# Performance work log

Hardware: AMD Instinct MI355X
Metric: run time of the kernel (lower is better)

The kernel has to match this reference:

```python
import jax, jax.numpy as jnp
import numpy as np

EPS = 1e-06        # normalize eps and log eps (module's self.eps)
PDIST_EPS = 1e-06  # torch.nn.PairwiseDistance default eps: ||x1 - x2 + eps||_2

A, C, F = 4096, 8, 64


def setup_inputs() -> dict:
    key = jax.random.key(0)
    x = jax.random.normal(key, (A, C, F), dtype=jnp.float32)
    return {"x": x}


def reference(x) -> jnp.ndarray:
    a = x.shape[0]
    c = x.shape[1]
    # F.normalize(p=2, dim=-1, eps=EPS): x / max(||x||_2, eps)
    nrm = jnp.linalg.norm(x, axis=-1, keepdims=True)
    xn = x / jnp.maximum(nrm, EPS)
    # pairwise cosine similarity per group: [C, A, A]
    sim = jnp.einsum('acf,bcf->cab', xn, xn)
    # mask self-similarity on the diagonal with -1
    diag = jnp.eye(a, dtype=bool)[None, :, :]
    sim = jnp.where(diag, -1.0, sim)
    # nearest neighbor per (c, a): argmax over b -> [C, A] -> [A, C]
    idx = jnp.argmax(sim, axis=-1).T
    # gather matched embeddings: x_match[a, c, f] = xn[idx[a, c], c, f]
    x_match = xn[idx, jnp.arange(c)[None, :], :]
    # PairwiseDistance(p=2, eps=1e-6): ||x - x_match + eps||_2 over last dim
    min_dist = jnp.linalg.norm(xn - x_match + PDIST_EPS, axis=-1)
    loss = -jnp.mean(jnp.log(min_dist + EPS))
    return loss
```

## Files before the change

kernel.cpp:

```cpp
#include <hip/hip_runtime.h>
#include <math.h>

#define AN 4096
#define CN 8
#define FN 64
#define ACN (AN*CN)

typedef __attribute__((ext_vector_type(8))) short bf16x8;
typedef __attribute__((ext_vector_type(4))) float f32x4;

#define GLL16(gsrc, ldst) \
    __builtin_amdgcn_global_load_lds( \
        (const __attribute__((address_space(1))) void*)(gsrc), \
        (__attribute__((address_space(3))) void*)(ldst), 16, 0, 0)

__device__ inline unsigned short f2bf(float f) {
    unsigned u = __float_as_uint(f);
    unsigned r = ((u >> 16) & 1) + 0x7FFFu;
    return (unsigned short)((u + r) >> 16);
}

__global__ __launch_bounds__(256) void k1_normalize(const float* __restrict__ x,
                                                    unsigned short* __restrict__ xnb,
                                                    float* __restrict__ inv)
{
    int tid  = threadIdx.x;
    int grp  = tid >> 4;
    int slot = tid & 15;
    #pragma unroll
    for (int s = 0; s < 4; ++s) {
        int V = blockIdx.x * 64 + s * 16 + grp;
        const float4 v = *(const float4*)(x + (size_t)V * FN + slot * 4);
        float ss = v.x*v.x + v.y*v.y + v.z*v.z + v.w*v.w;
        ss += __shfl_xor(ss, 1);
        ss += __shfl_xor(ss, 2);
        ss += __shfl_xor(ss, 4);
        ss += __shfl_xor(ss, 8);
        float sc = 1.0f / fmaxf(sqrtf(ss), 1e-6f);
        int a = V >> 3, c = V & 7;
        ushort4 ob;
        ob.x = f2bf(v.x * sc); ob.y = f2bf(v.y * sc);
        ob.z = f2bf(v.z * sc); ob.w = f2bf(v.w * sc);
        *(ushort4*)(xnb + ((size_t)c * AN + a) * FN + slot * 4) = ob;
        if (slot == 0) inv[V] = sc;
    }
}

__global__ __launch_bounds__(256, 2) void k2_argmax(const unsigned short* __restrict__ xnb,
                                                    unsigned int* __restrict__ pP)
{
    __shared__ uint4 lds4[3 * 1024];

    int blk  = blockIdx.x;
    int half = blk & 1;
    int rt   = (blk >> 1) & 31;
    int c    = blk >> 6;
    int a0   = rt * 128;
    int b0base = half * 2048;

    const char* __restrict__ Xc = (const char*)(xnb + (size_t)c * AN * FN);

    int tid  = threadIdx.x;
    int lane = tid & 63;
    int w    = tid >> 6;
    int l15  = lane & 15;
    int quad = lane >> 4;

    int srow  = lane >> 3;
    int sslot = lane & 7;

    #pragma unroll
    for (int s = 0; s < 4; ++s) {
        int base = (w * 4 + s) * 64;
        int row  = (base >> 3) + srow;
        int gch  = sslot ^ (row & 7);
        size_t gb = (size_t)row * 128 + (size_t)gch * 16;
        GLL16(Xc + (size_t)(a0) * 128 + gb,      lds4 + base);
        GLL16(Xc + (size_t)(b0base) * 128 + gb,  lds4 + 1024 + base);
    }
    __syncthreads();

    bf16x8 afr[8][2];
    #pragma unroll
    for (int mi = 0; mi < 8; ++mi)
        #pragma unroll
        for (int ks = 0; ks < 2; ++ks) {
            int r  = mi * 16 + l15;
            int ch = (ks * 4 + quad) ^ (r & 7);
            afr[mi][ks] = ((const bf16x8*)lds4)[r * 8 + ch];
        }

    float bestp[32];
    #pragma unroll
    for (int i = 0; i < 32; ++i) bestp[i] = 0.0f;

    const f32x4 two = {2.0f, 2.0f, 2.0f, 2.0f};

    for (int it = 0; it < 16; ++it) {
        int cur = it & 1;

        if (it < 15) {
            int g0 = b0base + (it + 1) * 128;
            #pragma unroll
            for (int s = 0; s < 4; ++s) {
                int base = (w * 4 + s) * 64;
                int row  = (base >> 3) + srow;
                int gch  = sslot ^ (row & 7);
                GLL16(Xc + (size_t)(g0 + row) * 128 + (size_t)gch * 16,
                      lds4 + 1024 + (cur ^ 1) * 1024 + base);
            }
        }

        f32x4 acc[8][2];
        const bf16x8* bt = (const bf16x8*)(lds4 + 1024 + cur * 1024);
        #pragma unroll
        for (int ks = 0; ks < 2; ++ks) {
            #pragma unroll
            for (int ni = 0; ni < 2; ++ni) {
                int r  = w * 32 + ni * 16 + l15;
                int ch = (ks * 4 + quad) ^ (r & 7);
                bf16x8 bfr = bt[r * 8 + ch];
                #pragma unroll
                for (int mi = 0; mi < 8; ++mi)
                    acc[mi][ni] = __builtin_amdgcn_mfma_f32_16x16x32_bf16(
                        afr[mi][ks], bfr, (ks == 0) ? two : acc[mi][ni], 0, 0, 0);
            }
        }

        int colblk = b0base + it * 128 + w * 32;
        #pragma unroll
        for (int mi = 0; mi < 8; ++mi) {
            int rfrag = a0 + mi * 16;
            #pragma unroll
            for (int r = 0; r < 4; ++r) {
                unsigned p0 = (__float_as_uint(acc[mi][0][r]) & 0xFFFFF000u)
                            | (unsigned)(colblk + l15);
                unsigned p1 = (__float_as_uint(acc[mi][1][r]) & 0xFFFFF000u)
                            | (unsigned)(colblk + 16 + l15);
                float c0 = __uint_as_float(p0);
                float c1 = __uint_as_float(p1);
                if (rfrag == colblk) {
                    if (l15 == quad * 4 + r) c0 = 0.0f;
                }
                if (rfrag == colblk + 16) {
                    if (l15 == quad * 4 + r) c1 = 0.0f;
                }
                int bi = mi * 4 + r;
                bestp[bi] = fmaxf(fmaxf(c0, c1), bestp[bi]);
            }
        }

        __syncthreads();
    }

    #pragma unroll
    for (int i = 0; i < 32; ++i) {
        float v = bestp[i];
        v = fmaxf(v, __shfl_xor(v, 1));
        v = fmaxf(v, __shfl_xor(v, 2));
        v = fmaxf(v, __shfl_xor(v, 4));
        v = fmaxf(v, __shfl_xor(v, 8));
        bestp[i] = v;
    }
    __syncthreads();
    float* red = (float*)lds4;
    if (l15 == 0) {
        #pragma unroll
        for (int mi = 0; mi < 8; ++mi)
            #pragma unroll
            for (int r = 0; r < 4; ++r)
                red[w * 128 + mi * 16 + quad * 4 + r] = bestp[mi * 4 + r];
    }
    __syncthreads();
    if (tid < 128) {
        float p = fmaxf(fmaxf(red[tid], red[128 + tid]),
                        fmaxf(red[256 + tid], red[384 + tid]));
        int a = a0 + tid;
        pP[(size_t)half * ACN + (size_t)a * CN + c] = __float_as_uint(p);
    }
}

__global__ __launch_bounds__(256) void k3_dist(const float* __restrict__ x,
                                               const float* __restrict__ inv,
                                               const unsigned int* __restrict__ pP,
                                               float* __restrict__ partials)
{
    int tid = threadIdx.x;
    int id = blockIdx.x * 256 + tid;
    float p0 = __uint_as_float(pP[id]);
    float p1 = __uint_as_float(pP[ACN + id]);
    unsigned pm = __float_as_uint(fmaxf(p0, p1));
    int m = (int)(pm & 0xFFFu);
    int c = id & 7;
    int idb = m * CN + c;
    float sa = inv[id];
    float sb = inv[idb];
    const float* xa = x + (size_t)id  * FN;
    const float* xb = x + (size_t)idb * FN;
    float ss = 0.0f;
    #pragma unroll
    for (int q = 0; q < 16; ++q) {
        float4 va = *(const float4*)(xa + 4 * q);
        float4 vb = *(const float4*)(xb + 4 * q);
        float d0 = va.x * sa - vb.x * sb + 1e-6f;
        float d1 = va.y * sa - vb.y * sb + 1e-6f;
        float d2 = va.z * sa - vb.z * sb + 1e-6f;
        float d3 = va.w * sa - vb.w * sb + 1e-6f;
        ss += d0*d0 + d1*d1 + d2*d2 + d3*d3;
    }
    float val = logf(sqrtf(ss) + 1e-6f);

    float t = val;
    #pragma unroll
    for (int off = 32; off > 0; off >>= 1) t += __shfl_down(t, off);
    __shared__ float ws4[4];
    if ((tid & 63) == 0) ws4[tid >> 6] = t;
    __syncthreads();
    if (tid == 0)
        partials[blockIdx.x] = ws4[0] + ws4[1] + ws4[2] + ws4[3];
}

__global__ __launch_bounds__(64) void k4_final(const float* __restrict__ partials,
                                               float* __restrict__ out)
{
    int t = threadIdx.x;
    float v = partials[t] + partials[t + 64];
    #pragma unroll
    for (int off = 32; off > 0; off >>= 1) v += __shfl_down(v, off);
    if (t == 0) out[0] = -v / (float)ACN;
}

extern "C" void kernel_launch(void* const* d_in, const int* in_sizes, int n_in,
                              void* d_out, int out_size, void* d_ws, size_t ws_size,
                              hipStream_t stream)
{
    const float* x = (const float*)d_in[0];
    unsigned short* xnb = (unsigned short*)d_ws;
    float* inv = (float*)(xnb + (size_t)AN * CN * FN);
    unsigned int* pP = (unsigned int*)(inv + ACN);
    float* partials = (float*)(pP + 2 * ACN);

    k1_normalize<<<512, 256, 0, stream>>>(x, xnb, inv);
    k2_argmax  <<<512, 256, 0, stream>>>(xnb, pP);
    k3_dist    <<<128, 256, 0, stream>>>(x, inv, pP, partials);
    k4_final   <<<1, 64, 0, stream>>>(partials, (float*)d_out);
}
```

Before: 94.56 us.

## Use per-wave 4-stage LDS ring for B tiles and drop per-iteration barriers

The argmax kernel changes from a block-wide double-buffered B tile to a 4-deep ring. Each wave now stages only the 32 B rows it consumes itself, tracked with explicit vmcnt waits, so the per-iteration __syncthreads can be removed. The loop is fully unrolled and the swizzled LDS addresses are precomputed. The aim is to hide global-load latency and cut barrier stalls. In exchange, LDS use rises to 80KB per block, which could limit occupancy, and code size grows.

Result: no change. 93.28 us (-1.3%).

```diff
diff --git a/kernel.cpp b/kernel.cpp
--- a/kernel.cpp
+++ b/kernel.cpp
@@ -49,7 +49,7 @@
 __global__ __launch_bounds__(256, 2) void k2_argmax(const unsigned short* __restrict__ xnb,
                                                     unsigned int* __restrict__ pP)
 {
-    __shared__ uint4 lds4[3 * 1024];
+    __shared__ char ldsc[5 * 16384];
 
     int blk  = blockIdx.x;
     int half = blk & 1;
@@ -65,30 +65,32 @@
     int w    = tid >> 6;
     int l15  = lane & 15;
     int quad = lane >> 4;
-
-    int srow  = lane >> 3;
+    int srow = lane >> 3;
     int sslot = lane & 7;
 
-    #pragma unroll
-    for (int s = 0; s < 4; ++s) {
-        int base = (w * 4 + s) * 64;
-        int row  = (base >> 3) + srow;
-        int gch  = sslot ^ (row & 7);
-        size_t gb = (size_t)row * 128 + (size_t)gch * 16;
-        GLL16(Xc + (size_t)(a0) * 128 + gb,      lds4 + base);
-        GLL16(Xc + (size_t)(b0base) * 128 + gb,  lds4 + 1024 + base);
-    }
-    __syncthreads();
-
+    int gl_lane = srow * 128 + ((sslot ^ srow) << 4);
+    const char* gA = Xc + (size_t)(a0 + w * 32) * 128 + gl_lane;
+    const char* gB = Xc + (size_t)(b0base + w * 32) * 128 + gl_lane;
+    char* ldsA = ldsc + w * 4096;
+    char* ldsB = ldsc + 16384 + w * 4096;
+
+    GLL16(gA,        ldsA);
+    GLL16(gA + 1024, ldsA + 1024);
+    GLL16(gA + 2048, ldsA + 2048);
+    GLL16(gA + 3072, ldsA + 3072);
+    __syncthreads();
+
+    int ab0 = l15 * 128 + ((quad ^ (l15 & 7)) << 4);
+    int ab1 = ab0 ^ 64;
     bf16x8 afr[8][2];
     #pragma unroll
-    for (int mi = 0; mi < 8; ++mi)
-        #pragma unroll
-        for (int ks = 0; ks < 2; ++ks) {
-            int r  = mi * 16 + l15;
-            int ch = (ks * 4 + quad) ^ (r & 7);
-            afr[mi][ks] = ((const bf16x8*)lds4)[r * 8 + ch];
-        }
+    for (int mi = 0; mi < 8; ++mi) {
+        afr[mi][0] = *(const bf16x8*)(ldsc + ab0 + mi * 2048);
+        afr[mi][1] = *(const bf16x8*)(ldsc + ab1 + mi * 2048);
+    }
+
+    int rb0 = 16384 + (w * 32 + l15) * 128 + ((quad ^ (l15 & 7)) << 4);
+    int rb1 = rb0 ^ 64;
 
     float bestp[32];
     #pragma unroll
@@ -96,30 +98,36 @@
 
     const f32x4 two = {2.0f, 2.0f, 2.0f, 2.0f};
 
+#define STAGE_B(IT) do { \
+        const char* _g = gB + (size_t)(IT) * 16384; \
+        char* _l = ldsB + ((IT) & 3) * 16384; \
+        GLL16(_g,        _l); \
+        GLL16(_g + 1024, _l + 1024); \
+        GLL16(_g + 2048, _l + 2048); \
+        GLL16(_g + 3072, _l + 3072); \
+    } while (0)
+
+    STAGE_B(0);
+    STAGE_B(1);
+    STAGE_B(2);
+
+    #pragma unroll
     for (int it = 0; it < 16; ++it) {
-        int cur = it & 1;
-
-        if (it < 15) {
-            int g0 = b0base + (it + 1) * 128;
-            #pragma unroll
-            for (int s = 0; s < 4; ++s) {
-                int base = (w * 4 + s) * 64;
-                int row  = (base >> 3) + srow;
-                int gch  = sslot ^ (row & 7);
-                GLL16(Xc + (size_t)(g0 + row) * 128 + (size_t)gch * 16,
-                      lds4 + 1024 + (cur ^ 1) * 1024 + base);
-            }
-        }
+        if (it <= 12) STAGE_B(it + 3);
+
+        if (it <= 12)      { asm volatile("s_waitcnt vmcnt(12)" ::: "memory"); }
+        else if (it == 13) { asm volatile("s_waitcnt vmcnt(8)"  ::: "memory"); }
+        else if (it == 14) { asm volatile("s_waitcnt vmcnt(4)"  ::: "memory"); }
+        else               { asm volatile("s_waitcnt vmcnt(0)"  ::: "memory"); }
+
+        const int bo = (it & 3) * 16384;
 
         f32x4 acc[8][2];
-        const bf16x8* bt = (const bf16x8*)(lds4 + 1024 + cur * 1024);
         #pragma unroll
         for (int ks = 0; ks < 2; ++ks) {
             #pragma unroll
             for (int ni = 0; ni < 2; ++ni) {
-                int r  = w * 32 + ni * 16 + l15;
-                int ch = (ks * 4 + quad) ^ (r & 7);
-                bf16x8 bfr = bt[r * 8 + ch];
+                bf16x8 bfr = *(const bf16x8*)(ldsc + (ks ? rb1 : rb0) + bo + ni * 2048);
                 #pragma unroll
                 for (int mi = 0; mi < 8; ++mi)
                     acc[mi][ni] = __builtin_amdgcn_mfma_f32_16x16x32_bf16(
@@ -149,9 +157,8 @@
                 bestp[bi] = fmaxf(fmaxf(c0, c1), bestp[bi]);
             }
         }
-
-        __syncthreads();
-    }
+    }
+#undef STAGE_B
 
     #pragma unroll
     for (int i = 0; i < 32; ++i) {
@@ -163,7 +170,7 @@
         bestp[i] = v;
     }
     __syncthreads();
-    float* red = (float*)lds4;
+    float* red = (float*)ldsc;
     if (l15 == 0) {
         #pragma unroll
         for (int mi = 0; mi < 8; ++mi)
```
